# Kernel optimization log

Hardware: AMD Instinct MI355X
Metric: run time of the kernel (lower is better)

The kernel has to match this reference:

```python
import jax, jax.numpy as jnp
import numpy as np
from jax import lax

EMBED = 768
D_INNER = 2 * EMBED          # expand = 2
D_STATE = 16
D_CONV = 4
DT_RANK = (EMBED + 15) // 16  # 48
FF = 3072
B, L = 2, 1024


def setup_inputs() -> dict:
    key = jax.random.key(0)
    ks = jax.random.split(key, 20)
    s = 0.02
    inp = {
        "x": jax.random.normal(ks[0], (B, L, EMBED), jnp.float32),
        # Mamba params
        "in_proj_w": jax.random.normal(ks[1], (2 * D_INNER, EMBED), jnp.float32) * s,
        "conv_w": jax.random.normal(ks[2], (D_INNER, 1, D_CONV), jnp.float32) * s,
        "conv_b": jnp.zeros((D_INNER,), jnp.float32),
        "x_proj_w": jax.random.normal(ks[3], (DT_RANK + 2 * D_STATE, D_INNER), jnp.float32) * s,
        "dt_proj_w": jax.random.normal(ks[4], (D_INNER, DT_RANK), jnp.float32) * s,
        "dt_proj_b": jax.random.normal(ks[5], (D_INNER,), jnp.float32) * s,
        "A_log": jnp.log(jnp.broadcast_to(jnp.arange(1, D_STATE + 1, dtype=jnp.float32), (D_INNER, D_STATE))),
        "D_param": jnp.ones((D_INNER,), jnp.float32),
        "out_proj_w": jax.random.normal(ks[6], (EMBED, D_INNER), jnp.float32) * s,
        # block params
        "ln1_w": jnp.ones((EMBED,), jnp.float32), "ln1_b": jnp.zeros((EMBED,), jnp.float32),
        "ln2_w": jnp.ones((EMBED,), jnp.float32), "ln2_b": jnp.zeros((EMBED,), jnp.float32),
        "ffn_w1": jax.random.normal(ks[7], (FF, EMBED), jnp.float32) * s,
        "ffn_b1": jnp.zeros((FF,), jnp.float32),
        "ffn_w2": jax.random.normal(ks[8], (EMBED, FF), jnp.float32) * s,
        "ffn_b2": jnp.zeros((EMBED,), jnp.float32),
    }
    return inp


def _layernorm(x, w, b, eps=1e-5):
    mu = jnp.mean(x, -1, keepdims=True)
    var = jnp.mean((x - mu) ** 2, -1, keepdims=True)
    return (x - mu) * lax.rsqrt(var + eps) * w + b


def _mamba(x, in_proj_w, conv_w, conv_b, x_proj_w, dt_proj_w, dt_proj_b,
           A_log, D_param, out_proj_w):
    # x: [B, L, E]
    xz = jnp.einsum('ble,de->bld', x, in_proj_w)          # [B,L,2*Di]
    xin, z = jnp.split(xz, 2, axis=-1)                    # [B,L,Di] each
    # causal depthwise conv over time
    xc = lax.conv_general_dilated(
        xin.transpose(0, 2, 1), conv_w, window_strides=(1,),
        padding=[(D_CONV - 1, 0)], feature_group_count=D_INNER,
        dimension_numbers=('NCH', 'OIH', 'NCH'))
    xc = (xc + conv_b[None, :, None]).transpose(0, 2, 1)  # [B,L,Di]
    xc = jax.nn.silu(xc)
    # input-dependent SSM params
    x_dbl = jnp.einsum('bld,rd->blr', xc, x_proj_w)       # [B,L,dt_rank+2n]
    dt, Bm, Cm = jnp.split(x_dbl, [DT_RANK, DT_RANK + D_STATE], axis=-1)
    delta = jax.nn.softplus(jnp.einsum('blr,dr->bld', dt, dt_proj_w) + dt_proj_b)
    A = -jnp.exp(A_log)                                   # [Di, n]
    deltaA = jnp.exp(jnp.einsum('bld,dn->bldn', delta, A))
    deltaBu = jnp.einsum('bld,bln,bld->bldn', delta, Bm, xc)

    def step(h, xs):
        dA, dBu, Ct = xs                                  # [B,Di,n],[B,Di,n],[B,n]
        h = dA * h + dBu
        y = jnp.einsum('bdn,bn->bd', h, Ct)
        return h, y

    h0 = jnp.zeros((x.shape[0], D_INNER, D_STATE), x.dtype)
    _, ys = lax.scan(step, h0, (deltaA.transpose(1, 0, 2, 3),
                                deltaBu.transpose(1, 0, 2, 3),
                                Cm.transpose(1, 0, 2)))
    y = ys.transpose(1, 0, 2)                             # [B,L,Di]
    y = y + xc * D_param
    y = y * jax.nn.silu(z)
    return jnp.einsum('bld,ed->ble', y, out_proj_w)


def reference(x, in_proj_w, conv_w, conv_b, x_proj_w, dt_proj_w, dt_proj_b,
              A_log, D_param, out_proj_w, ln1_w, ln1_b, ln2_w, ln2_b,
              ffn_w1, ffn_b1, ffn_w2, ffn_b2):
    # dropout is identity in eval mode
    h = _mamba(x, in_proj_w, conv_w, conv_b, x_proj_w, dt_proj_w, dt_proj_b,
               A_log, D_param, out_proj_w)
    x1 = _layernorm(h + x, ln1_w, ln1_b)
    f = jnp.einsum('ble,fe->blf', x1, ffn_w1) + ffn_b1
    f = jax.nn.gelu(f)
    f = jnp.einsum('blf,ef->ble', f, ffn_w2) + ffn_b2
    return _layernorm(f + x1, ln2_w, ln2_b)
```

## Files before the change

### kernel.cpp

```cpp
#include <hip/hip_runtime.h>
#include <math.h>

#define EMBED 768
#define DI 1536
#define DSTATE 16
#define DCONV 4
#define DTRANK 48
#define FF 3072
#define BATCH 2
#define SEQ 1024
#define NROWS (BATCH*SEQ)
#define TCH 32
#define NCH (SEQ/TCH)
#define DBLK 64

typedef __bf16 bf16x8 __attribute__((ext_vector_type(8)));
typedef float f32x4 __attribute__((ext_vector_type(4)));
typedef unsigned int u32x4 __attribute__((ext_vector_type(4)));

static __device__ __forceinline__ unsigned short f2b(float f) {
    union { float f; unsigned u; } v; v.f = f;
    unsigned r = v.u + 0x7FFFu + ((v.u >> 16) & 1u);
    return (unsigned short)(r >> 16);
}
static __device__ __forceinline__ float b2f(unsigned short s) {
    union { unsigned u; float f; } v; v.u = ((unsigned)s) << 16;
    return v.f;
}

#define GLOAD_LDS16(g, l) __builtin_amdgcn_global_load_lds( \
    (const __attribute__((address_space(1))) void*)(g), \
    (__attribute__((address_space(3))) void*)(l), 16, 0, 0)

template<int EPI, int KSPLIT>
__global__ __launch_bounds__(256)
void gemm_b(const unsigned short* __restrict__ A,
            const unsigned short* __restrict__ W,
            float* __restrict__ C, unsigned short* __restrict__ Cb,
            float* __restrict__ part,
            int M, int N, int K,
            const float* __restrict__ bias)
{
    __shared__ alignas(16) unsigned short As[128 * 32];
    __shared__ alignas(16) unsigned short Ws[128 * 32];
    const int tid  = threadIdx.x;
    const int lane = tid & 63, wave = tid >> 6;
    const int wr = (wave >> 1) * 64, wc = (wave & 1) * 64;
    const int bm = blockIdx.y * 128, bn = blockIdx.x * 128;
    const int kc = K / KSPLIT;
    const int kz = blockIdx.z * kc;
    const int ln = lane & 15, lg = lane >> 4;

    f32x4 acc[4][4];
    #pragma unroll
    for (int i = 0; i < 4; ++i)
        #pragma unroll
        for (int j = 0; j < 4; ++j)
            acc[i][j] = (f32x4){0.f, 0.f, 0.f, 0.f};

    const int ra = tid >> 2, ca = tid & 3;
    const int cs = (ca * 8) ^ ((ra & 3) << 3);
    const unsigned short* gA0 = A + (size_t)(bm + ra) * K + kz + cs;
    const unsigned short* gA1 = A + (size_t)(bm + ra + 64) * K + kz + cs;
    const unsigned short* gW0 = W + (size_t)(bn + ra) * K + kz + cs;
    const unsigned short* gW1 = W + (size_t)(bn + ra + 64) * K + kz + cs;
    unsigned short* ldsA0 = As + wave * 512;
    unsigned short* ldsA1 = As + 2048 + wave * 512;
    unsigned short* ldsW0 = Ws + wave * 512;
    unsigned short* ldsW1 = Ws + 2048 + wave * 512;

    for (int k0 = 0; k0 < kc; k0 += 32) {
        GLOAD_LDS16(gA0 + k0, ldsA0);
        GLOAD_LDS16(gA1 + k0, ldsA1);
        GLOAD_LDS16(gW0 + k0, ldsW0);
        GLOAD_LDS16(gW1 + k0, ldsW1);
        __syncthreads();
        bf16x8 af[4], wf[4];
        #pragma unroll
        for (int i = 0; i < 4; ++i) {
            int row = wr + i * 16 + ln;
            af[i] = *reinterpret_cast<const bf16x8*>(
                &As[row * 32 + ((lg * 8) ^ ((row & 3) << 3))]);
        }
        #pragma unroll
        for (int j = 0; j < 4; ++j) {
            int row = wc + j * 16 + ln;
            wf[j] = *reinterpret_cast<const bf16x8*>(
                &Ws[row * 32 + ((lg * 8) ^ ((row & 3) << 3))]);
        }
        #pragma unroll
        for (int i = 0; i < 4; ++i)
            #pragma unroll
            for (int j = 0; j < 4; ++j)
                acc[i][j] = __builtin_amdgcn_mfma_f32_16x16x32_bf16(af[i], wf[j], acc[i][j], 0, 0, 0);
        __syncthreads();
    }

    if constexpr (KSPLIT > 1) {
        float* pb = part + (size_t)blockIdx.z * M * N;
        #pragma unroll
        for (int i = 0; i < 4; ++i)
            #pragma unroll
            for (int j = 0; j < 4; ++j) {
                int col = bn + wc + j * 16 + ln;
                #pragma unroll
                for (int rr = 0; rr < 4; ++rr) {
                    int row = bm + wr + i * 16 + lg * 4 + rr;
                    pb[(size_t)row * N + col] = acc[i][j][rr];
                }
            }
    } else {
        #pragma unroll
        for (int i = 0; i < 4; ++i)
            #pragma unroll
            for (int j = 0; j < 4; ++j) {
                int col = bn + wc + j * 16 + ln;
                #pragma unroll
                for (int rr = 0; rr < 4; ++rr) {
                    int row = bm + wr + i * 16 + lg * 4 + rr;
                    float v = acc[i][j][rr];
                    size_t o = (size_t)row * N + col;
                    if (EPI == 1) {
                        v += bias[col];
                        C[o] = (v > 20.f) ? v : log1pf(expf(v));
                    } else if (EPI == 3) {
                        v += bias[col];
                        float t = 0.7978845608028654f * (v + 0.044715f * v * v * v);
                        Cb[o] = f2b(0.5f * v * (1.f + tanhf(t)));
                    } else if (EPI == 5) {
                        if (col < DI) C[(size_t)row * DI + col] = v;
                        else          Cb[(size_t)row * DI + col - DI] = f2b(v);
                    } else {
                        C[o] = v;
                    }
                }
            }
    }
}

template<int KS, int BIAS>
__global__ __launch_bounds__(256)
void reduce_ln(const float* __restrict__ part, const float* __restrict__ resid,
               const float* __restrict__ bias,
               const float* __restrict__ w, const float* __restrict__ bb,
               float* __restrict__ out, unsigned short* __restrict__ outb)
{
    const int row = blockIdx.x;
    const size_t ro = (size_t)row * EMBED;
    const int i0 = threadIdx.x, i1 = i0 + 256, i2 = i0 + 512;
    float v0 = 0.f, v1 = 0.f, v2 = 0.f;
    #pragma unroll
    for (int z = 0; z < KS; ++z) {
        const float* p = part + (size_t)z * NROWS * EMBED + ro;
        v0 += p[i0]; v1 += p[i1]; v2 += p[i2];
    }
    if (BIAS) { v0 += bias[i0]; v1 += bias[i1]; v2 += bias[i2]; }
    v0 += resid[ro + i0]; v1 += resid[ro + i1]; v2 += resid[ro + i2];

    float s  = v0 + v1 + v2;
    float s2 = v0 * v0 + v1 * v1 + v2 * v2;
    #pragma unroll
    for (int m = 1; m < 64; m <<= 1) {
        s  += __shfl_xor(s,  m);
        s2 += __shfl_xor(s2, m);
    }
    __shared__ float sh1[4], sh2[4];
    int wv = threadIdx.x >> 6;
    if ((threadIdx.x & 63) == 0) { sh1[wv] = s; sh2[wv] = s2; }
    __syncthreads();
    float S1 = sh1[0] + sh1[1] + sh1[2] + sh1[3];
    float S2 = sh2[0] + sh2[1] + sh2[2] + sh2[3];
    float mu  = S1 * (1.f / EMBED);
    float var = S2 * (1.f / EMBED) - mu * mu;
    float rs  = rsqrtf(var + 1e-5f);
    float o0 = (v0 - mu) * rs * w[i0] + bb[i0];
    float o1 = (v1 - mu) * rs * w[i1] + bb[i1];
    float o2 = (v2 - mu) * rs * w[i2] + bb[i2];
    out[ro + i0] = o0; out[ro + i1] = o1; out[ro + i2] = o2;
    if (outb) {
        outb[ro + i0] = f2b(o0); outb[ro + i1] = f2b(o1); outb[ro + i2] = f2b(o2);
    }
}

__global__ __launch_bounds__(256)
void xproj_mfma(const unsigned short* __restrict__ A,
                const unsigned short* __restrict__ W,
                float* __restrict__ part)
{
    const int mt = blockIdx.x, s = blockIdx.y;
    const int lane = threadIdx.x & 63, wave = threadIdx.x >> 6;
    const int ln = lane & 15, lg = lane >> 4;
    const int row0 = mt * 128 + wave * 32;
    const int kb = s * 192;
    f32x4 acc[2][5];
    #pragma unroll
    for (int i = 0; i < 2; ++i)
        #pragma unroll
        for (int j = 0; j < 5; ++j)
            acc[i][j] = (f32x4){0.f, 0.f, 0.f, 0.f};

    for (int kk = 0; kk < 192; kk += 32) {
        const int k = kb + kk + lg * 8;
        bf16x8 af[2], wf[5];
        af[0] = *reinterpret_cast<const bf16x8*>(A + (size_t)(row0 + ln) * DI + k);
        af[1] = *reinterpret_cast<const bf16x8*>(A + (size_t)(row0 + 16 + ln) * DI + k);
        #pragma unroll
        for (int j = 0; j < 5; ++j)
            wf[j] = *reinterpret_cast<const bf16x8*>(W + (size_t)(j * 16 + ln) * DI + k);
        #pragma unroll
        for (int i = 0; i < 2; ++i)
            #pragma unroll
            for (int j = 0; j < 5; ++j)
                acc[i][j] = __builtin_amdgcn_mfma_f32_16x16x32_bf16(af[i], wf[j], acc[i][j], 0, 0, 0);
    }
    float* pb = part + (size_t)s * NROWS * 80;
    #pragma unroll
    for (int i = 0; i < 2; ++i)
        #pragma unroll
        for (int j = 0; j < 5; ++j)
            #pragma unroll
            for (int rr = 0; rr < 4; ++rr) {
                int row = row0 + i * 16 + lg * 4 + rr;
                int col = j * 16 + ln;
                pb[(size_t)row * 80 + col] = acc[i][j][rr];
            }
}

__global__ __launch_bounds__(256)
void xproj_reduce(const float* __restrict__ part, float* __restrict__ xdbl,
                  unsigned short* __restrict__ xdblb)
{
    int idx = blockIdx.x * 256 + threadIdx.x;
    float sum = 0.f;
    #pragma unroll
    for (int s = 0; s < 8; ++s) sum += part[(size_t)s * NROWS * 80 + idx];
    xdbl[idx] = sum;
    int col = idx % 80, row = idx / 80;
    if (col < 48)      xdblb[row * 64 + col] = f2b(sum);
    else if (col < 64) xdblb[row * 64 + col] = 0;
}

__global__ __launch_bounds__(256)
void cvt7_k(const float* __restrict__ x,  const float* __restrict__ w1,
            const float* __restrict__ w2, const float* __restrict__ w3,
            const float* __restrict__ w4, const float* __restrict__ w5,
            const float* __restrict__ w6,
            unsigned short* __restrict__ xb,  unsigned short* __restrict__ w1b,
            unsigned short* __restrict__ w2b, unsigned short* __restrict__ w3b,
            unsigned short* __restrict__ w4b, unsigned short* __restrict__ w5b,
            unsigned short* __restrict__ w6b)
{
    size_t i4 = ((size_t)blockIdx.x * 256 + threadIdx.x) * 4;
    if (i4 >= 9953280u) {
        int off = (int)(i4 - 9953280u);
        if (off >= 98304) return;
        int row = off >> 6, colb = off & 63;
        ushort4 u = {0, 0, 0, 0};
        if (colb < 48) {
            float4 v = *reinterpret_cast<const float4*>(w6 + row * 48 + colb);
            u.x = f2b(v.x); u.y = f2b(v.y); u.z = f2b(v.z); u.w = f2b(v.w);
        }
        *reinterpret_cast<ushort4*>(w6b + off) = u;
        return;
    }
    const float* src; unsigned short* dst; size_t off;
    if      (i4 < 1572864u) { src = x;  dst = xb;  off = i4; }
    else if (i4 < 3932160u) { src = w1; dst = w1b; off = i4 - 1572864u; }
    else if (i4 < 5111808u) { src = w2; dst = w2b; off = i4 - 3932160u; }
    else if (i4 < 7471104u) { src = w3; dst = w3b; off = i4 - 5111808u; }
    else if (i4 < 9830400u) { src = w4; dst = w4b; off = i4 - 7471104u; }
    else                    { src = w5; dst = w5b; off = i4 - 9830400u; }
    float4 v = *reinterpret_cast<const float4*>(src + off);
    ushort4 u;
    u.x = f2b(v.x); u.y = f2b(v.y); u.z = f2b(v.z); u.w = f2b(v.w);
    *reinterpret_cast<ushort4*>(dst + off) = u;
}

__global__ __launch_bounds__(256)
void conv_silu_k(const float* __restrict__ xin, const float* __restrict__ cw,
                 const float* __restrict__ cb, float* __restrict__ xc,
                 unsigned short* __restrict__ xcb)
{
    int q = blockIdx.x * 256 + threadIdx.x;
    int d4 = (q * 4) % DI;
    int bt = (q * 4) / DI;
    int t  = bt % SEQ;
    const float* base = xin + (size_t)bt * DI + d4;
    float4 s3 = *reinterpret_cast<const float4*>(base);
    float4 acc = *reinterpret_cast<const float4*>(cb + d4);
    float4 wv0 = *reinterpret_cast<const float4*>(cw + (d4 + 0) * 4);
    float4 wv1 = *reinterpret_cast<const float4*>(cw + (d4 + 1) * 4);
    float4 wv2 = *reinterpret_cast<const float4*>(cw + (d4 + 2) * 4);
    float4 wv3 = *reinterpret_cast<const float4*>(cw + (d4 + 3) * 4);
    acc.x += wv0.w * s3.x; acc.y += wv1.w * s3.y; acc.z += wv2.w * s3.z; acc.w += wv3.w * s3.w;
    if (t >= 1) {
        float4 s = *reinterpret_cast<const float4*>(base - DI);
        acc.x += wv0.z * s.x; acc.y += wv1.z * s.y; acc.z += wv2.z * s.z; acc.w += wv3.z * s.w;
    }
    if (t >= 2) {
        float4 s = *reinterpret_cast<const float4*>(base - 2 * DI);
        acc.x += wv0.y * s.x; acc.y += wv1.y * s.y; acc.z += wv2.y * s.z; acc.w += wv3.y * s.w;
    }
    if (t >= 3) {
        float4 s = *reinterpret_cast<const float4*>(base - 3 * DI);
        acc.x += wv0.x * s.x; acc.y += wv1.x * s.y; acc.z += wv2.x * s.z; acc.w += wv3.x * s.w;
    }
    float4 v;
    v.x = acc.x / (1.f + __expf(-acc.x));
    v.y = acc.y / (1.f + __expf(-acc.y));
    v.z = acc.z / (1.f + __expf(-acc.z));
    v.w = acc.w / (1.f + __expf(-acc.w));
    size_t o = (size_t)bt * DI + d4;
    *reinterpret_cast<float4*>(xc + o) = v;
    ushort4 u; u.x = f2b(v.x); u.y = f2b(v.y); u.z = f2b(v.z); u.w = f2b(v.w);
    *reinterpret_cast<ushort4*>(xcb + o) = u;
}

__global__ __launch_bounds__(256)
void scan2_a(const float* __restrict__ delta, const float* __restrict__ xc,
             const float* __restrict__ xdbl,  const float* __restrict__ A_log,
             float* __restrict__ hfin, float* __restrict__ aprod)
{
    const int d0 = blockIdx.x * DBLK, ch = blockIdx.y, b = blockIdx.z;
    const int t0 = ch * TCH;
    __shared__ float del_s[TCH][DBLK + 4];
    __shared__ float xc_s[TCH][DBLK + 4];
    __shared__ float b_s[TCH][20];
    const int tid = threadIdx.x;
    {
        const int c4 = tid & 15, tr = tid >> 4;
        #pragma unroll
        for (int p = 0; p < 2; ++p) {
            int t = p * 16 + tr;
            size_t rowo = (size_t)(b * SEQ + t0 + t);
            *reinterpret_cast<float4*>(&del_s[t][c4 * 4]) =
                *reinterpret_cast<const float4*>(&delta[rowo * DI + d0 + c4 * 4]);
            *reinterpret_cast<float4*>(&xc_s[t][c4 * 4]) =
                *reinterpret_cast<const float4*>(&xc[rowo * DI + d0 + c4 * 4]);
        }
        const int cbq = tid & 3, tb = tid >> 2;
        if (tb < TCH) {
            size_t rowo = (size_t)(b * SEQ + t0 + tb);
            *reinterpret_cast<float4*>(&b_s[tb][cbq * 4]) =
                *reinterpret_cast<const float4*>(&xdbl[rowo * 80 + DTRANK + cbq * 4]);
        }
    }
    __syncthreads();
    const int lane = tid & 63, wave = tid >> 6;
    const int wd = wave * 16 + (lane >> 2);
    const int d = d0 + wd;
    const int nq = (lane & 3) * 4;
    float4 Av = *reinterpret_cast<const float4*>(&A_log[d * DSTATE + nq]);
    const float A0 = -__expf(Av.x), A1 = -__expf(Av.y), A2 = -__expf(Av.z), A3 = -__expf(Av.w);
    float h0_ = 0.f, h1_ = 0.f, h2_ = 0.f, h3_ = 0.f;
    float p0 = 1.f, p1 = 1.f, p2 = 1.f, p3 = 1.f;
    #pragma unroll 4
    for (int t = 0; t < TCH; ++t) {
        float dl = del_s[t][wd];
        float u  = dl * xc_s[t][wd];
        float4 bq = *reinterpret_cast<const float4*>(&b_s[t][nq]);
        float e0 = __expf(dl * A0), e1 = __expf(dl * A1);
        float e2 = __expf(dl * A2), e3 = __expf(dl * A3);
        h0_ = e0 * h0_ + u * bq.x; p0 *= e0;
        h1_ = e1 * h1_ + u * bq.y; p1 *= e1;
        h2_ = e2 * h2_ + u * bq.z; p2 *= e2;
        h3_ = e3 * h3_ + u * bq.w; p3 *= e3;
    }
    size_t o = ((size_t)((b * NCH + ch) * DI) + d) * DSTATE + nq;
    *reinterpret_cast<float4*>(&hfin[o])  = (float4){h0_, h1_, h2_, h3_};
    *reinterpret_cast<float4*>(&aprod[o]) = (float4){p0, p1, p2, p3};
}

__global__ __launch_bounds__(256)
void scan2_c(const float* __restrict__ delta, const float* __restrict__ xc,
             const float* __restrict__ xdbl,  const float* __restrict__ A_log,
             const float* __restrict__ Dp,    const unsigned short* __restrict__ zb,
             const float* __restrict__ hfin,  const float* __restrict__ aprod,
             unsigned short* __restrict__ yb)
{
    const int d0 = blockIdx.x * DBLK, ch = blockIdx.y, b = blockIdx.z;
    const int t0 = ch * TCH;
    __shared__ float del_s[TCH][DBLK + 4];
    __shared__ float xc_s[TCH][DBLK + 4];
    __shared__ float b_s[TCH][20];
    __shared__ float c_s[TCH][20];
    __shared__ unsigned short z_s[TCH][DBLK + 8];
    const int tid = threadIdx.x;
    {
        const int c4 = tid & 15, tr = tid >> 4;
        #pragma unroll
        for (int p = 0; p < 2; ++p) {
            int t = p * 16 + tr;
            size_t rowo = (size_t)(b * SEQ + t0 + t);
            *reinterpret_cast<float4*>(&del_s[t][c4 * 4]) =
                *reinterpret_cast<const float4*>(&delta[rowo * DI + d0 + c4 * 4]);
            *reinterpret_cast<float4*>(&xc_s[t][c4 * 4]) =
                *reinterpret_cast<const float4*>(&xc[rowo * DI + d0 + c4 * 4]);
        }
        const int cbq = tid & 3, tb = tid >> 2;
        if (tb < TCH) {
            size_t rowo = (size_t)(b * SEQ + t0 + tb);
            *reinterpret_cast<float4*>(&b_s[tb][cbq * 4]) =
                *reinterpret_cast<const float4*>(&xdbl[rowo * 80 + DTRANK + cbq * 4]);
        } else {
            size_t rowo = (size_t)(b * SEQ + t0 + tb - TCH);
            *reinterpret_cast<float4*>(&c_s[tb - TCH][cbq * 4]) =
                *reinterpret_cast<const float4*>(&xdbl[rowo * 80 + DTRANK + DSTATE + cbq * 4]);
        }
        const int cz = tid & 7, tz = tid >> 3;
        size_t rz = (size_t)(b * SEQ + t0 + tz);
        *reinterpret_cast<u32x4*>(&z_s[tz][cz * 8]) =
            *reinterpret_cast<const u32x4*>(&zb[rz * DI + d0 + cz * 8]);
    }
    const int lane = tid & 63, wave = tid >> 6;
    const int wd = wave * 16 + (lane >> 2);
    const int d = d0 + wd;
    const int nq = (lane & 3) * 4;

    float4 h = {0.f, 0.f, 0.f, 0.f};
    for (int cc = 0; cc < ch; ++cc) {
        size_t o = ((size_t)((b * NCH + cc) * DI) + d) * DSTATE + nq;
        float4 a = *reinterpret_cast<const float4*>(&aprod[o]);
        float4 f = *reinterpret_cast<const float4*>(&hfin[o]);
        h.x = a.x * h.x + f.x; h.y = a.y * h.y + f.y;
        h.z = a.z * h.z + f.z; h.w = a.w * h.w + f.w;
    }

    float4 Av = *reinterpret_cast<const float4*>(&A_log[d * DSTATE + nq]);
    const float A0 = -__expf(Av.x), A1 = -__expf(Av.y), A2 = -__expf(Av.z), A3 = -__expf(Av.w);
    const float Dd = Dp[d];
    __syncthreads();
    unsigned short* yrow = yb + (size_t)(b * SEQ + t0) * DI + d;
    #pragma unroll 4
    for (int t = 0; t < TCH; ++t) {
        float dl = del_s[t][wd];
        float xv = xc_s[t][wd];
        float u  = dl * xv;
        float4 bq = *reinterpret_cast<const float4*>(&b_s[t][nq]);
        float4 cq = *reinterpret_cast<const float4*>(&c_s[t][nq]);
        float e0 = __expf(dl * A0), e1 = __expf(dl * A1);
        float e2 = __expf(dl * A2), e3 = __expf(dl * A3);
        h.x = e0 * h.x + u * bq.x;
        h.y = e1 * h.y + u * bq.y;
        h.z = e2 * h.z + u * bq.z;
        h.w = e3 * h.w + u * bq.w;
        float py = h.x * cq.x + h.y * cq.y + h.z * cq.z + h.w * cq.w;
        py += __shfl_xor(py, 1);
        py += __shfl_xor(py, 2);
        if ((lane & 3) == 0) {
            float yv = py + xv * Dd;
            float zv = b2f(z_s[t][wd]);
            yv *= zv / (1.f + __expf(-zv));
            yrow[(size_t)t * DI] = f2b(yv);
        }
    }
}

extern "C" void kernel_launch(void* const* d_in, const int* in_sizes, int n_in,
                              void* d_out, int out_size, void* d_ws, size_t ws_size,
                              hipStream_t stream)
{
    const float* x         = (const float*)d_in[0];
    const float* in_proj_w = (const float*)d_in[1];
    const float* conv_w    = (const float*)d_in[2];
    const float* conv_b    = (const float*)d_in[3];
    const float* x_proj_w  = (const float*)d_in[4];
    const float* dt_proj_w = (const float*)d_in[5];
    const float* dt_proj_b = (const float*)d_in[6];
    const float* A_log     = (const float*)d_in[7];
    const float* D_param   = (const float*)d_in[8];
    const float* out_proj_w= (const float*)d_in[9];
    const float* ln1_w     = (const float*)d_in[10];
    const float* ln1_b     = (const float*)d_in[11];
    const float* ln2_w     = (const float*)d_in[12];
    const float* ln2_b     = (const float*)d_in[13];
    const float* ffn_w1    = (const float*)d_in[14];
    const float* ffn_b1    = (const float*)d_in[15];
    const float* ffn_w2    = (const float*)d_in[16];
    const float* ffn_b2    = (const float*)d_in[17];
    float* out = (float*)d_out;

    char* Wp = (char*)d_ws;
    float*          xin   = (float*)         (Wp + 0);
    unsigned short* zbuf  = (unsigned short*)(Wp + 12582912);
    float*          xc    = (float*)         (Wp + 18874368);
    float*          xdbl  = (float*)         (Wp + 31457280);
    float*          delta = (float*)         (Wp + 32112640);
    unsigned short* ybb   = (unsigned short*)(Wp + 44695552);
    unsigned short* xb    = (unsigned short*)(Wp + 58851328);
    unsigned short* wib   = (unsigned short*)(Wp + 61997056);
    unsigned short* wob   = (unsigned short*)(Wp + 66715648);
    unsigned short* wf1b  = (unsigned short*)(Wp + 69074944);
    unsigned short* wf2b  = (unsigned short*)(Wp + 73793536);
    unsigned short* fbf   = (unsigned short*)(Wp + 0);
    float*          x1    = (float*)         (Wp + 32112640);
    unsigned short* x1b   = (unsigned short*)(Wp + 58851328);
    float*          part  = (float*)         (Wp + 0);
    unsigned short* xdblb = (unsigned short*)(Wp + 5242880);
    unsigned short* xcb   = (unsigned short*)(Wp + 58851328);
    unsigned short* xpwb  = (unsigned short*)(Wp + 50987008);
    unsigned short* wdtb  = (unsigned short*)(Wp + 51232768);
    float*          hfin  = (float*)         (Wp + 0);
    float*          aprod = (float*)         (Wp + 6291456);
    float*          part_op = (float*)       (Wp + 0);
    float*          part_f2 = (float*)       (Wp + 38404096);

    dim3 blk(256);

    cvt7_k<<<9816, blk, 0, stream>>>(x, in_proj_w, out_proj_w, ffn_w1, ffn_w2, x_proj_w,
                                     dt_proj_w, xb, wib, wob, wf1b, wf2b, xpwb, wdtb);

    gemm_b<5, 1><<<dim3(24, 16, 1), blk, 0, stream>>>(xb, wib, xin, zbuf, nullptr,
                                                      NROWS, 2 * DI, EMBED, nullptr);

    conv_silu_k<<<(BATCH * SEQ * DI) / 1024, blk, 0, stream>>>(xin, conv_w, conv_b, xc, xcb);

    xproj_mfma<<<dim3(16, 8), blk, 0, stream>>>(xcb, xpwb, part);
    xproj_reduce<<<640, blk, 0, stream>>>(part, xdbl, xdblb);

    gemm_b<1, 1><<<dim3(12, 16, 1), blk, 0, stream>>>(xdblb, wdtb, delta, nullptr, nullptr,
                                                      NROWS, DI, 64, dt_proj_b);

    scan2_a<<<dim3(DI / DBLK, NCH, BATCH), blk, 0, stream>>>(delta, xc, xdbl, A_log, hfin, aprod);
    scan2_c<<<dim3(DI / DBLK, NCH, BATCH), blk, 0, stream>>>(delta, xc, xdbl, A_log, D_param,
                                                             zbuf, hfin, aprod, ybb);

    gemm_b<0, 4><<<dim3(6, 16, 4), blk, 0, stream>>>(ybb, wob, nullptr, nullptr, part_op,
                                                     NROWS, EMBED, DI, nullptr);
    reduce_ln<4, 0><<<NROWS, blk, 0, stream>>>(part_op, x, nullptr, ln1_w, ln1_b, x1, x1b);

    gemm_b<3, 1><<<dim3(24, 16, 1), blk, 0, stream>>>(x1b, wf1b, nullptr, fbf, nullptr,
                                                      NROWS, FF, EMBED, ffn_b1);

    gemm_b<0, 4><<<dim3(6, 16, 4), blk, 0, stream>>>(fbf, wf2b, nullptr, nullptr, part_f2,
                                                     NROWS, EMBED, FF, nullptr);
    reduce_ln<4, 1><<<NROWS, blk, 0, stream>>>(part_f2, x1, ffn_b2, ln2_w, ln2_b, out, nullptr);
}
```

Measured before the change: 229.9 us.

## Shrink GEMM tile to 128x64 and add separate inter-chunk scan carry kernel

All GEMMs now use a 128x64 block tile with each wave computing 32x64, which doubles the grid to improve CU occupancy on small problems at the cost of less operand reuse per block. Separately, the sequential carry-in over previous chunks, which each scan2_c block used to recompute with O(ch) global reads, is moved into a new scan2_b kernel. scan2_b computes every chunk's initial state once and writes it to a buffer that scan2_c reads directly. This adds one small kernel launch and reuses a workspace region for h0.

Measured after the change: 208.5 us. -9.3%, faster.

```diff
diff --git a/kernel.cpp b/kernel.cpp
--- a/kernel.cpp
+++ b/kernel.cpp
@@ -34,26 +34,25 @@
 
 template<int EPI, int KSPLIT>
 __global__ __launch_bounds__(256)
-void gemm_b(const unsigned short* __restrict__ A,
-            const unsigned short* __restrict__ W,
-            float* __restrict__ C, unsigned short* __restrict__ Cb,
-            float* __restrict__ part,
-            int M, int N, int K,
-            const float* __restrict__ bias)
+void gemm_sk(const unsigned short* __restrict__ A,
+             const unsigned short* __restrict__ W,
+             float* __restrict__ C, unsigned short* __restrict__ Cb,
+             float* __restrict__ part,
+             int M, int N, int K,
+             const float* __restrict__ bias)
 {
     __shared__ alignas(16) unsigned short As[128 * 32];
-    __shared__ alignas(16) unsigned short Ws[128 * 32];
+    __shared__ alignas(16) unsigned short Ws[64 * 32];
     const int tid  = threadIdx.x;
     const int lane = tid & 63, wave = tid >> 6;
-    const int wr = (wave >> 1) * 64, wc = (wave & 1) * 64;
-    const int bm = blockIdx.y * 128, bn = blockIdx.x * 128;
+    const int bm = blockIdx.y * 128, bn = blockIdx.x * 64;
     const int kc = K / KSPLIT;
     const int kz = blockIdx.z * kc;
     const int ln = lane & 15, lg = lane >> 4;
 
-    f32x4 acc[4][4];
-    #pragma unroll
-    for (int i = 0; i < 4; ++i)
+    f32x4 acc[2][4];
+    #pragma unroll
+    for (int i = 0; i < 2; ++i)
         #pragma unroll
         for (int j = 0; j < 4; ++j)
             acc[i][j] = (f32x4){0.f, 0.f, 0.f, 0.f};
@@ -62,34 +61,31 @@
     const int cs = (ca * 8) ^ ((ra & 3) << 3);
     const unsigned short* gA0 = A + (size_t)(bm + ra) * K + kz + cs;
     const unsigned short* gA1 = A + (size_t)(bm + ra + 64) * K + kz + cs;
-    const unsigned short* gW0 = W + (size_t)(bn + ra) * K + kz + cs;
-    const unsigned short* gW1 = W + (size_t)(bn + ra + 64) * K + kz + cs;
+    const unsigned short* gW  = W + (size_t)(bn + ra) * K + kz + cs;
     unsigned short* ldsA0 = As + wave * 512;
     unsigned short* ldsA1 = As + 2048 + wave * 512;
-    unsigned short* ldsW0 = Ws + wave * 512;
-    unsigned short* ldsW1 = Ws + 2048 + wave * 512;
+    unsigned short* ldsW  = Ws + wave * 512;
 
     for (int k0 = 0; k0 < kc; k0 += 32) {
         GLOAD_LDS16(gA0 + k0, ldsA0);
         GLOAD_LDS16(gA1 + k0, ldsA1);
-        GLOAD_LDS16(gW0 + k0, ldsW0);
-        GLOAD_LDS16(gW1 + k0, ldsW1);
+        GLOAD_LDS16(gW  + k0, ldsW);
         __syncthreads();
-        bf16x8 af[4], wf[4];
-        #pragma unroll
-        for (int i = 0; i < 4; ++i) {
-            int row = wr + i * 16 + ln;
+        bf16x8 af[2], wf[4];
+        #pragma unroll
+        for (int i = 0; i < 2; ++i) {
+            int row = wave * 32 + i * 16 + ln;
             af[i] = *reinterpret_cast<const bf16x8*>(
                 &As[row * 32 + ((lg * 8) ^ ((row & 3) << 3))]);
         }
         #pragma unroll
         for (int j = 0; j < 4; ++j) {
-            int row = wc + j * 16 + ln;
+            int row = j * 16 + ln;
             wf[j] = *reinterpret_cast<const bf16x8*>(
                 &Ws[row * 32 + ((lg * 8) ^ ((row & 3) << 3))]);
         }
         #pragma unroll
-        for (int i = 0; i < 4; ++i)
+        for (int i = 0; i < 2; ++i)
             #pragma unroll
             for (int j = 0; j < 4; ++j)
                 acc[i][j] = __builtin_amdgcn_mfma_f32_16x16x32_bf16(af[i], wf[j], acc[i][j], 0, 0, 0);
@@ -99,25 +95,25 @@
     if constexpr (KSPLIT > 1) {
         float* pb = part + (size_t)blockIdx.z * M * N;
         #pragma unroll
-        for (int i = 0; i < 4; ++i)
+        for (int i = 0; i < 2; ++i)
             #pragma unroll
             for (int j = 0; j < 4; ++j) {
-                int col = bn + wc + j * 16 + ln;
+                int col = bn + j * 16 + ln;
                 #pragma unroll
                 for (int rr = 0; rr < 4; ++rr) {
-                    int row = bm + wr + i * 16 + lg * 4 + rr;
+                    int row = bm + wave * 32 + i * 16 + lg * 4 + rr;
                     pb[(size_t)row * N + col] = acc[i][j][rr];
                 }
             }
     } else {
         #pragma unroll
-        for (int i = 0; i < 4; ++i)
+        for (int i = 0; i < 2; ++i)
             #pragma unroll
             for (int j = 0; j < 4; ++j) {
-                int col = bn + wc + j * 16 + ln;
+                int col = bn + j * 16 + ln;
                 #pragma unroll
                 for (int rr = 0; rr < 4; ++rr) {
-                    int row = bm + wr + i * 16 + lg * 4 + rr;
+                    int row = bm + wave * 32 + i * 16 + lg * 4 + rr;
                     float v = acc[i][j][rr];
                     size_t o = (size_t)row * N + col;
                     if (EPI == 1) {
@@ -372,10 +368,30 @@
 }
 
 __global__ __launch_bounds__(256)
+void scan2_b(const float* __restrict__ hfin, const float* __restrict__ aprod,
+             float* __restrict__ h0)
+{
+    int idx = blockIdx.x * 256 + threadIdx.x;
+    int nq = (idx & 3) * 4;
+    int d  = (idx >> 2) % DI;
+    int b  = (idx >> 2) / DI;
+    float4 h = {0.f, 0.f, 0.f, 0.f};
+    #pragma unroll
+    for (int ch = 0; ch < NCH; ++ch) {
+        size_t o = ((size_t)((b * NCH + ch) * DI) + d) * DSTATE + nq;
+        *reinterpret_cast<float4*>(&h0[o]) = h;
+        float4 a = *reinterpret_cast<const float4*>(&aprod[o]);
+        float4 f = *reinterpret_cast<const float4*>(&hfin[o]);
+        h.x = a.x * h.x + f.x; h.y = a.y * h.y + f.y;
+        h.z = a.z * h.z + f.z; h.w = a.w * h.w + f.w;
+    }
+}
+
+__global__ __launch_bounds__(256)
 void scan2_c(const float* __restrict__ delta, const float* __restrict__ xc,
              const float* __restrict__ xdbl,  const float* __restrict__ A_log,
              const float* __restrict__ Dp,    const unsigned short* __restrict__ zb,
-             const float* __restrict__ hfin,  const float* __restrict__ aprod,
+             const float* __restrict__ h0,
              unsigned short* __restrict__ yb)
 {
     const int d0 = blockIdx.x * DBLK, ch = blockIdx.y, b = blockIdx.z;
@@ -412,24 +428,16 @@
         *reinterpret_cast<u32x4*>(&z_s[tz][cz * 8]) =
             *reinterpret_cast<const u32x4*>(&zb[rz * DI + d0 + cz * 8]);
     }
+    __syncthreads();
     const int lane = tid & 63, wave = tid >> 6;
     const int wd = wave * 16 + (lane >> 2);
     const int d = d0 + wd;
     const int nq = (lane & 3) * 4;
-
-    float4 h = {0.f, 0.f, 0.f, 0.f};
-    for (int cc = 0; cc < ch; ++cc) {
-        size_t o = ((size_t)((b * NCH + cc) * DI) + d) * DSTATE + nq;
-        float4 a = *reinterpret_cast<const float4*>(&aprod[o]);
-        float4 f = *reinterpret_cast<const float4*>(&hfin[o]);
-        h.x = a.x * h.x + f.x; h.y = a.y * h.y + f.y;
-        h.z = a.z * h.z + f.z; h.w = a.w * h.w + f.w;
-    }
-
     float4 Av = *reinterpret_cast<const float4*>(&A_log[d * DSTATE + nq]);
     const float A0 = -__expf(Av.x), A1 = -__expf(Av.y), A2 = -__expf(Av.z), A3 = -__expf(Av.w);
     const float Dd = Dp[d];
-    __syncthreads();
+    float4 h = *reinterpret_cast<const float4*>(
+        &h0[((size_t)((b * NCH + ch) * DI) + d) * DSTATE + nq]);
     unsigned short* yrow = yb + (size_t)(b * SEQ + t0) * DI + d;
     #pragma unroll 4
     for (int t = 0; t < TCH; ++t) {
@@ -502,6 +510,7 @@
     unsigned short* wdtb  = (unsigned short*)(Wp + 51232768);
     float*          hfin  = (float*)         (Wp + 0);
     float*          aprod = (float*)         (Wp + 6291456);
+    float*          h0    = (float*)         (Wp + 50987008);
     float*          part_op = (float*)       (Wp + 0);
     float*          part_f2 = (float*)       (Wp + 38404096);
 
@@ -510,29 +519,30 @@
     cvt7_k<<<9816, blk, 0, stream>>>(x, in_proj_w, out_proj_w, ffn_w1, ffn_w2, x_proj_w,
                                      dt_proj_w, xb, wib, wob, wf1b, wf2b, xpwb, wdtb);
 
-    gemm_b<5, 1><<<dim3(24, 16, 1), blk, 0, stream>>>(xb, wib, xin, zbuf, nullptr,
-                                                      NROWS, 2 * DI, EMBED, nullptr);
+    gemm_sk<5, 1><<<dim3(48, 16, 1), blk, 0, stream>>>(xb, wib, xin, zbuf, nullptr,
+                                                       NROWS, 2 * DI, EMBED, nullptr);
 
     conv_silu_k<<<(BATCH * SEQ * DI) / 1024, blk, 0, stream>>>(xin, conv_w, conv_b, xc, xcb);
 
     xproj_mfma<<<dim3(16, 8), blk, 0, stream>>>(xcb, xpwb, part);
     xproj_reduce<<<640, blk, 0, stream>>>(part, xdbl, xdblb);
 
-    gemm_b<1, 1><<<dim3(12, 16, 1), blk, 0, stream>>>(xdblb, wdtb, delta, nullptr, nullptr,
-                                                      NROWS, DI, 64, dt_proj_b);
+    gemm_sk<1, 1><<<dim3(24, 16, 1), blk, 0, stream>>>(xdblb, wdtb, delta, nullptr, nullptr,
+                                                       NROWS, DI, 64, dt_proj_b);
 
     scan2_a<<<dim3(DI / DBLK, NCH, BATCH), blk, 0, stream>>>(delta, xc, xdbl, A_log, hfin, aprod);
+    scan2_b<<<48, blk, 0, stream>>>(hfin, aprod, h0);
     scan2_c<<<dim3(DI / DBLK, NCH, BATCH), blk, 0, stream>>>(delta, xc, xdbl, A_log, D_param,
-                                                             zbuf, hfin, aprod, ybb);
-
-    gemm_b<0, 4><<<dim3(6, 16, 4), blk, 0, stream>>>(ybb, wob, nullptr, nullptr, part_op,
-                                                     NROWS, EMBED, DI, nullptr);
+                                                             zbuf, h0, ybb);
+
+    gemm_sk<0, 4><<<dim3(12, 16, 4), blk, 0, stream>>>(ybb, wob, nullptr, nullptr, part_op,
+                                                       NROWS, EMBED, DI, nullptr);
     reduce_ln<4, 0><<<NROWS, blk, 0, stream>>>(part_op, x, nullptr, ln1_w, ln1_b, x1, x1b);
 
-    gemm_b<3, 1><<<dim3(24, 16, 1), blk, 0, stream>>>(x1b, wf1b, nullptr, fbf, nullptr,
-                                                      NROWS, FF, EMBED, ffn_b1);
-
-    gemm_b<0, 4><<<dim3(6, 16, 4), blk, 0, stream>>>(fbf, wf2b, nullptr, nullptr, part_f2,
-                                                     NROWS, EMBED, FF, nullptr);
+    gemm_sk<3, 1><<<dim3(48, 16, 1), blk, 0, stream>>>(x1b, wf1b, nullptr, fbf, nullptr,
+                                                       NROWS, FF, EMBED, ffn_b1);
+
+    gemm_sk<0, 4><<<dim3(12, 16, 4), blk, 0, stream>>>(fbf, wf2b, nullptr, nullptr, part_f2,
+                                                       NROWS, EMBED, FF, nullptr);
     reduce_ln<4, 1><<<NROWS, blk, 0, stream>>>(part_f2, x1, ffn_b2, ln2_w, ln2_b, out, nullptr);
 }
```
